# Kernel tuning notes

Hardware: AMD Instinct MI355X
Metric: run time of the kernel (lower is better)

## Reference

```python
import jax, jax.numpy as jnp
import numpy as np

N = 50000        # nodes
E = 300000       # edges
D_IN = 256
D_H = 256
D_OUT = 64       # num classes
L = 3            # num GAT layers
G = 500          # num graphs in batch
NEG_SLOPE = 0.2


def setup_inputs() -> dict:
    key = jax.random.key(0)
    ks = jax.random.split(key, 12)
    x = jax.random.normal(ks[0], (N, D_IN), dtype=jnp.float32)
    edge_index = jax.random.randint(ks[1], (2, E), 0, N, dtype=jnp.int64)
    batch = jnp.sort(jax.random.randint(ks[2], (N,), 0, G, dtype=jnp.int64))
    # GAT layer params (all layers same width since D_IN == D_H)
    Ws = jax.random.normal(ks[3], (L, D_H, D_H), dtype=jnp.float32) * 0.05
    atts = jax.random.normal(ks[4], (L, 2 * D_H, 1), dtype=jnp.float32) * 0.05
    bs = jnp.zeros((L, D_H), dtype=jnp.float32)
    # post_mp: Linear(D_H,D_H) -> Dropout(0) -> Linear(D_H,D_OUT)
    pW1 = jax.random.normal(ks[5], (D_H, D_H), dtype=jnp.float32) * 0.05
    pb1 = jnp.zeros((D_H,), dtype=jnp.float32)
    pW2 = jax.random.normal(ks[6], (D_OUT, D_H), dtype=jnp.float32) * 0.05
    pb2 = jnp.zeros((D_OUT,), dtype=jnp.float32)
    return dict(x=x, edge_index=edge_index, batch=batch, Ws=Ws, atts=atts,
                bs=bs, pW1=pW1, pb1=pb1, pW2=pW2, pb2=pb2)


def _gat_layer(x, W, att, b, src, dst):
    h = x @ W.T                                   # [N, D_H] (lin, no bias)
    xi = h[dst]                                   # target features  [E, D_H]
    xj = h[src]                                   # source features  [E, D_H]
    e = jnp.concatenate([xi, xj], axis=1) @ att   # [E, 1]
    e = jax.nn.leaky_relu(e[:, 0], NEG_SLOPE)     # [E]
    # segment softmax keyed by destination node
    m = jax.ops.segment_max(e, dst, num_segments=N)
    m = jnp.where(jnp.isfinite(m), m, 0.0)        # empty segments -> 0
    ee = jnp.exp(e - m[dst])
    s = jax.ops.segment_sum(ee, dst, num_segments=N)
    alpha = ee / (s[dst] + 1e-16)                 # [E]
    # weighted scatter-add aggregation (aggr='add'); heads=1, concat view is identity
    out = jax.ops.segment_sum(alpha[:, None] * xj, dst, num_segments=N)
    return out + b


def reference(x, edge_index, batch, Ws, atts, bs, pW1, pb1, pW2, pb2):
    src = edge_index[0]
    dst = edge_index[1]
    for l in range(L):
        x = _gat_layer(x, Ws[l], atts[l], bs[l], src, dst)
    # Dropout(p=0) is identity
    x = jax.nn.relu(x)
    g = jax.ops.segment_max(x, batch, num_segments=G)   # global_max_pool [G, D_H]
    h = g @ pW1.T + pb1
    out = h @ pW2.T + pb2
    return jax.nn.log_softmax(out, axis=1)
```

## Files before the change

### kernel.cpp

```cpp
#include <hip/hip_runtime.h>
#include <math.h>

#define NEG_SLOPE 0.2f

typedef __attribute__((ext_vector_type(8))) short s16x8;
typedef __attribute__((ext_vector_type(4))) float f32x4;
typedef unsigned short ushort_t;
typedef unsigned int uint_t;

__device__ inline ushort_t f2bf(float f) {
    unsigned u = __float_as_uint(f);
    unsigned r = (u + 0x7fff + ((u >> 16) & 1)) >> 16;
    return (ushort_t)r;
}
__device__ inline float bf2f(ushort_t u) {
    return __uint_as_float(((unsigned)u) << 16);
}

__global__ __launch_bounds__(256) void cvt_kernel(const float* __restrict__ in,
        ushort_t* __restrict__ out, int n4) {
    int i = blockIdx.x * 256 + threadIdx.x;
    if (i < n4) {
        float4 v = ((const float4*)in)[i];
        ushort4 o;
        o.x = f2bf(v.x); o.y = f2bf(v.y); o.z = f2bf(v.z); o.w = f2bf(v.w);
        ((ushort4*)out)[i] = o;
    }
}

__global__ void deg_kernel(const int* __restrict__ ei, int* __restrict__ deg, int E) {
    int e = blockIdx.x * blockDim.x + threadIdx.x;
    if (e < E) atomicAdd(&deg[ei[E + e]], 1);
}

__global__ __launch_bounds__(1024) void scan1(const int* __restrict__ deg,
        int* __restrict__ tscan, int* __restrict__ bsum, int n) {
    __shared__ int ws[16];
    int t = threadIdx.x;
    int gi = blockIdx.x * 1024 + t;
    int v = (gi < n) ? deg[gi] : 0;
    int lane = t & 63, w = t >> 6;
    int s = v;
#pragma unroll
    for (int off = 1; off < 64; off <<= 1) {
        int u = __shfl_up(s, off);
        if (lane >= off) s += u;
    }
    if (lane == 63) ws[w] = s;
    __syncthreads();
    if (w == 0) {
        int x = (lane < 16) ? ws[lane] : 0;
#pragma unroll
        for (int off = 1; off < 16; off <<= 1) {
            int u = __shfl_up(x, off);
            if (lane >= off) x += u;
        }
        if (lane < 16) ws[lane] = x;
    }
    __syncthreads();
    int woff = (w > 0) ? ws[w - 1] : 0;
    if (gi < n) tscan[gi] = woff + s - v;
    if (t == 1023) bsum[blockIdx.x] = woff + s;
}

__global__ void scan2(const int* __restrict__ bsum, int* __restrict__ boff,
                      int nb, int* __restrict__ total_out) {
    int lane = threadIdx.x;
    int v = (lane < nb) ? bsum[lane] : 0;
    int s = v;
#pragma unroll
    for (int off = 1; off < 64; off <<= 1) {
        int u = __shfl_up(s, off);
        if (lane >= off) s += u;
    }
    if (lane < nb) boff[lane] = s - v;
    if (lane == 63) *total_out = s;
}

__global__ __launch_bounds__(1024) void scan3(const int* __restrict__ tscan,
        const int* __restrict__ boff, int* __restrict__ rowptr,
        int* __restrict__ cursor, int n) {
    int i = blockIdx.x * 1024 + threadIdx.x;
    if (i < n) {
        int v = tscan[i] + boff[blockIdx.x];
        rowptr[i] = v;
        cursor[i] = v;
    }
}

__global__ void scatter_kernel(const int* __restrict__ ei, int* __restrict__ cursor,
                               int* __restrict__ adj, int E) {
    int e = blockIdx.x * blockDim.x + threadIdx.x;
    if (e < E) {
        int d = ei[E + e];
        int pos = atomicAdd(&cursor[d], 1);
        adj[pos] = ei[e];
    }
}

__global__ __launch_bounds__(256) void gemm_bf16(const ushort_t* __restrict__ A,
        const ushort_t* __restrict__ B, ushort_t* __restrict__ C,
        const float* __restrict__ att, float* __restrict__ a_dst,
        float* __restrict__ a_src, int n) {
    __shared__ ushort_t As[128 * 32];
    __shared__ ushort_t Bs[128 * 32];
    const int t = threadIdx.x;
    const int lane = t & 63, wid = t >> 6;
    const int wr = wid >> 1, wc = wid & 1;
    const long brow = (long)blockIdx.x * 128;
    const int bcol = blockIdx.y * 128;

    f32x4 acc[4][4] = {};

    const int r0 = wid * 16 + (lane >> 2);
    const int kof = (lane & 3) * 8;
    const int fr = lane & 15, kg = lane >> 4;

    for (int kt = 0; kt < 256; kt += 32) {
        __builtin_amdgcn_global_load_lds(
            (const __attribute__((address_space(1))) void*)(A + (brow + r0) * 256 + kt + kof),
            (__attribute__((address_space(3))) void*)(As + wid * 512 + lane * 8), 16, 0, 0);
        __builtin_amdgcn_global_load_lds(
            (const __attribute__((address_space(1))) void*)(A + (brow + r0 + 64) * 256 + kt + kof),
            (__attribute__((address_space(3))) void*)(As + (wid + 4) * 512 + lane * 8), 16, 0, 0);
        __builtin_amdgcn_global_load_lds(
            (const __attribute__((address_space(1))) void*)(B + (bcol + r0) * 256 + kt + kof),
            (__attribute__((address_space(3))) void*)(Bs + wid * 512 + lane * 8), 16, 0, 0);
        __builtin_amdgcn_global_load_lds(
            (const __attribute__((address_space(1))) void*)(B + (bcol + r0 + 64) * 256 + kt + kof),
            (__attribute__((address_space(3))) void*)(Bs + (wid + 4) * 512 + lane * 8), 16, 0, 0);
        asm volatile("s_waitcnt vmcnt(0)" ::: "memory");
        __syncthreads();

        s16x8 a[4], b[4];
#pragma unroll
        for (int m = 0; m < 4; m++)
            a[m] = *(const s16x8*)(As + (wr * 64 + m * 16 + fr) * 32 + kg * 8);
#pragma unroll
        for (int nn = 0; nn < 4; nn++)
            b[nn] = *(const s16x8*)(Bs + (wc * 64 + nn * 16 + fr) * 32 + kg * 8);
#pragma unroll
        for (int m = 0; m < 4; m++)
#pragma unroll
            for (int nn = 0; nn < 4; nn++)
                acc[m][nn] = __builtin_amdgcn_mfma_f32_16x16x32_bf16(a[m], b[nn], acc[m][nn], 0, 0, 0);
        __syncthreads();
    }

    const int rg = lane >> 4;
    const float* attL = att;
    const float* attR = att + 256;
#pragma unroll
    for (int m = 0; m < 4; m++) {
        long rbase = brow + wr * 64 + m * 16 + rg * 4;
#pragma unroll
        for (int r = 0; r < 4; r++) {
            long row = rbase + r;
            float sL = 0.f, sR = 0.f;
#pragma unroll
            for (int nn = 0; nn < 4; nn++) {
                int col = bcol + wc * 64 + nn * 16 + fr;
                float v = acc[m][nn][r];
                C[row * 256 + col] = f2bf(v);
                sL = fmaf(v, attL[col], sL);
                sR = fmaf(v, attR[col], sR);
            }
#pragma unroll
            for (int off = 8; off; off >>= 1) {
                sL += __shfl_xor(sL, off);
                sR += __shfl_xor(sR, off);
            }
            if (fr == 0 && row < n) {
                atomicAdd(&a_dst[row], sL);
                atomicAdd(&a_src[row], sR);
            }
        }
    }
}

__global__ __launch_bounds__(256) void gat_agg(const ushort_t* __restrict__ H,
        const float* __restrict__ a_dst, const float* __restrict__ a_src,
        const int* __restrict__ rowptr, const int* __restrict__ adj,
        const float* __restrict__ bias, ushort_t* __restrict__ OUTbf, int n) {
    int w = threadIdx.x >> 6, lane = threadIdx.x & 63;
    int node = blockIdx.x * 4 + w;
    if (node >= n) return;
    int beg = rowptr[node], end = rowptr[node + 1];
    float ai = a_dst[node];

    float m = -3.4e38f;
    for (int j = beg + lane; j < end; j += 64) {
        float e = ai + a_src[adj[j]];
        e = (e > 0.f) ? e : NEG_SLOPE * e;
        m = fmaxf(m, e);
    }
#pragma unroll
    for (int off = 32; off; off >>= 1) m = fmaxf(m, __shfl_xor(m, off));

    const int g = lane >> 4, fl = lane & 15;
    float ssum = 0.f;
    float acc[16];
#pragma unroll
    for (int k = 0; k < 16; k++) acc[k] = 0.f;

    for (int j0 = beg; j0 < end; j0 += 4) {
        int j = j0 + g;
        if (j < end) {
            int sidx = adj[j];
            float tt = ai + a_src[sidx];
            tt = (tt > 0.f) ? tt : NEG_SLOPE * tt;
            float wgt = expf(tt - m);
            ssum += wgt;
            const ushort_t* hp = H + (size_t)sidx * 256 + fl * 16;
            uint4 q0 = *(const uint4*)(hp);
            uint4 q1 = *(const uint4*)(hp + 8);
            uint_t qs[8] = {q0.x, q0.y, q0.z, q0.w, q1.x, q1.y, q1.z, q1.w};
#pragma unroll
            for (int k = 0; k < 8; k++) {
                float flo = __uint_as_float(qs[k] << 16);
                float fhi = __uint_as_float(qs[k] & 0xffff0000u);
                acc[2 * k]     = fmaf(wgt, flo, acc[2 * k]);
                acc[2 * k + 1] = fmaf(wgt, fhi, acc[2 * k + 1]);
            }
        }
    }

#pragma unroll
    for (int k = 0; k < 16; k++) {
        acc[k] += __shfl_xor(acc[k], 16);
        acc[k] += __shfl_xor(acc[k], 32);
    }
    ssum += __shfl_xor(ssum, 16);
    ssum += __shfl_xor(ssum, 32);

    if (g == 0) {
        float inv = 1.f / (ssum + 1e-16f);
        float bv[16];
        *(float4*)&bv[0]  = *(const float4*)(bias + fl * 16);
        *(float4*)&bv[4]  = *(const float4*)(bias + fl * 16 + 4);
        *(float4*)&bv[8]  = *(const float4*)(bias + fl * 16 + 8);
        *(float4*)&bv[12] = *(const float4*)(bias + fl * 16 + 12);
        uint_t ou[8];
#pragma unroll
        for (int k = 0; k < 8; k++) {
            uint_t lo = f2bf(acc[2 * k] * inv + bv[2 * k]);
            uint_t hi = f2bf(acc[2 * k + 1] * inv + bv[2 * k + 1]);
            ou[k] = lo | (hi << 16);
        }
        uint4* op = (uint4*)(OUTbf + (size_t)node * 256 + fl * 16);
        op[0] = make_uint4(ou[0], ou[1], ou[2], ou[3]);
        op[1] = make_uint4(ou[4], ou[5], ou[6], ou[7]);
    }
}

__global__ __launch_bounds__(1024) void pool_kernel(const ushort_t* __restrict__ X,
        const int* __restrict__ batch, float* __restrict__ gbuf, int n) {
    __shared__ float red[4][256];
    int g = blockIdx.x;
    int c = threadIdx.x & 255;
    int rg = threadIdx.x >> 8;
    int lo = 0, hi = n;
    while (lo < hi) { int mid = (lo + hi) >> 1; if (batch[mid] < g) lo = mid + 1; else hi = mid; }
    int start = lo;
    hi = n;
    while (lo < hi) { int mid = (lo + hi) >> 1; if (batch[mid] < g + 1) lo = mid + 1; else hi = mid; }
    int end_ = lo;
    float m = 0.f;
    for (int i = start + rg; i < end_; i += 4)
        m = fmaxf(m, bf2f(X[(size_t)i * 256 + c]));
    red[rg][c] = m;
    __syncthreads();
    if (rg == 0) {
        m = fmaxf(fmaxf(red[0][c], red[1][c]), fmaxf(red[2][c], red[3][c]));
        gbuf[g * 256 + c] = m;
    }
}

__global__ __launch_bounds__(256) void final_kernel(const float* __restrict__ gbuf,
        const float* __restrict__ pW1, const float* __restrict__ pb1,
        const float* __restrict__ pW2, const float* __restrict__ pb2,
        float* __restrict__ out) {
    __shared__ float gl[256];
    __shared__ float h1[256];
    int g = blockIdx.x, t = threadIdx.x;
    gl[t] = gbuf[g * 256 + t];
    __syncthreads();
    float acc = pb1[t];
    for (int k = 0; k < 256; k++) acc = fmaf(gl[k], pW1[t * 256 + k], acc);
    h1[t] = acc;
    __syncthreads();
    if (t < 64) {
        float o = pb2[t];
        for (int k = 0; k < 256; k++) o = fmaf(h1[k], pW2[t * 256 + k], o);
        float mx = o;
#pragma unroll
        for (int off = 32; off; off >>= 1) mx = fmaxf(mx, __shfl_xor(mx, off));
        float ex = expf(o - mx);
        float s = ex;
#pragma unroll
        for (int off = 32; off; off >>= 1) s += __shfl_xor(s, off);
        out[g * 64 + t] = o - mx - logf(s);
    }
}

extern "C" void kernel_launch(void* const* d_in, const int* in_sizes, int n_in,
                              void* d_out, int out_size, void* d_ws, size_t ws_size,
                              hipStream_t stream) {
    const float* x     = (const float*)d_in[0];
    const int*   ei    = (const int*)d_in[1];
    const int*   batch = (const int*)d_in[2];
    const float* Ws    = (const float*)d_in[3];
    const float* atts  = (const float*)d_in[4];
    const float* bs    = (const float*)d_in[5];
    const float* pW1   = (const float*)d_in[6];
    const float* pb1   = (const float*)d_in[7];
    const float* pW2   = (const float*)d_in[8];
    const float* pb2   = (const float*)d_in[9];
    float* out = (float*)d_out;

    const int N = in_sizes[0] / 256;
    const int E = in_sizes[1] / 2;
    const int G = out_size / 64;
    const int L = in_sizes[3] / (256 * 256);
    const int MB = (N + 127) / 128;
    const int Npad = MB * 128;
    const int NT = (N + 1023) / 1024;

    char* ws = (char*)d_ws;
    size_t off = 0;
    auto alloc = [&](size_t bytes) -> char* {
        char* p = ws + off;
        off += (bytes + 255) & ~size_t(255);
        return p;
    };
    ushort_t* Hbf    = (ushort_t*)alloc((size_t)Npad * 256 * 2);
    ushort_t* Xbf    = (ushort_t*)alloc((size_t)Npad * 256 * 2);
    ushort_t* Wbf    = (ushort_t*)alloc((size_t)L * 256 * 256 * 2);
    float*    a_both = (float*)alloc((size_t)2 * N * 4);
    float*    a_dst  = a_both;
    float*    a_src  = a_both + N;
    int*      deg    = (int*)alloc((size_t)N * 4);
    int*      rowptr = (int*)alloc((size_t)(N + 1) * 4);
    int*      cursor = (int*)alloc((size_t)N * 4);
    int*      adj    = (int*)alloc((size_t)E * 4);
    int*      tscan  = (int*)alloc((size_t)N * 4);
    int*      bsum   = (int*)alloc((size_t)64 * 4);
    int*      boff   = (int*)alloc((size_t)64 * 4);
    float*    gbuf   = (float*)alloc((size_t)G * 256 * 4);

    hipMemsetAsync(deg, 0, (size_t)N * 4, stream);
    int eb = (E + 255) / 256;
    deg_kernel<<<eb, 256, 0, stream>>>(ei, deg, E);
    scan1<<<NT, 1024, 0, stream>>>(deg, tscan, bsum, N);
    scan2<<<1, 64, 0, stream>>>(bsum, boff, NT, rowptr + N);
    scan3<<<NT, 1024, 0, stream>>>(tscan, boff, rowptr, cursor, N);
    scatter_kernel<<<eb, 256, 0, stream>>>(ei, cursor, adj, E);

    cvt_kernel<<<(N * 64 + 255) / 256, 256, 0, stream>>>(x, Xbf, N * 64);
    cvt_kernel<<<(L * 16384 + 255) / 256, 256, 0, stream>>>(Ws, Wbf, L * 16384);

    for (int l = 0; l < L; ++l) {
        hipMemsetAsync(a_both, 0, (size_t)2 * N * 4, stream);
        dim3 ggrid(MB, 2);
        gemm_bf16<<<ggrid, 256, 0, stream>>>(Xbf, Wbf + (size_t)l * 65536, Hbf,
                                             atts + (size_t)l * 512, a_dst, a_src, N);
        gat_agg<<<(N + 3) / 4, 256, 0, stream>>>(Hbf, a_dst, a_src, rowptr, adj,
                                                 bs + (size_t)l * 256, Xbf, N);
    }
    pool_kernel<<<G, 1024, 0, stream>>>(Xbf, batch, gbuf, N);
    final_kernel<<<G, 256, 0, stream>>>(gbuf, pW1, pb1, pW2, pb2, out);
}
```

Before: 368.3 us.

## Merge setup launches, drop per-layer memsets, cache edge scores for low-degree nodes

```diff
diff --git a/kernel.cpp b/kernel.cpp
--- a/kernel.cpp
+++ b/kernel.cpp
@@ -17,14 +17,21 @@
     return __uint_as_float(((unsigned)u) << 16);
 }
 
-__global__ __launch_bounds__(256) void cvt_kernel(const float* __restrict__ in,
-        ushort_t* __restrict__ out, int n4) {
+__global__ __launch_bounds__(256) void cvt2_kernel(const float* __restrict__ a,
+        ushort_t* __restrict__ oa, int na4,
+        const float* __restrict__ b, ushort_t* __restrict__ ob, int nb4) {
     int i = blockIdx.x * 256 + threadIdx.x;
-    if (i < n4) {
-        float4 v = ((const float4*)in)[i];
+    if (i < na4) {
+        float4 v = ((const float4*)a)[i];
         ushort4 o;
         o.x = f2bf(v.x); o.y = f2bf(v.y); o.z = f2bf(v.z); o.w = f2bf(v.w);
-        ((ushort4*)out)[i] = o;
+        ((ushort4*)oa)[i] = o;
+    } else if (i - na4 < nb4) {
+        int k = i - na4;
+        float4 v = ((const float4*)b)[k];
+        ushort4 o;
+        o.x = f2bf(v.x); o.y = f2bf(v.y); o.z = f2bf(v.z); o.w = f2bf(v.w);
+        ((ushort4*)ob)[k] = o;
     }
 }
 
@@ -63,28 +70,28 @@
     if (t == 1023) bsum[blockIdx.x] = woff + s;
 }
 
-__global__ void scan2(const int* __restrict__ bsum, int* __restrict__ boff,
-                      int nb, int* __restrict__ total_out) {
-    int lane = threadIdx.x;
-    int v = (lane < nb) ? bsum[lane] : 0;
-    int s = v;
-#pragma unroll
-    for (int off = 1; off < 64; off <<= 1) {
-        int u = __shfl_up(s, off);
-        if (lane >= off) s += u;
-    }
-    if (lane < nb) boff[lane] = s - v;
-    if (lane == 63) *total_out = s;
-}
-
 __global__ __launch_bounds__(1024) void scan3(const int* __restrict__ tscan,
-        const int* __restrict__ boff, int* __restrict__ rowptr,
-        int* __restrict__ cursor, int n) {
-    int i = blockIdx.x * 1024 + threadIdx.x;
+        const int* __restrict__ bsum, const int* __restrict__ deg,
+        int* __restrict__ rowptr, int* __restrict__ cursor, int n, int nb) {
+    __shared__ int sboff;
+    int t = threadIdx.x;
+    if (t < 64) {
+        int v = (t < nb) ? bsum[t] : 0;
+        int s = v;
+#pragma unroll
+        for (int off = 1; off < 64; off <<= 1) {
+            int u = __shfl_up(s, off);
+            if (t >= off) s += u;
+        }
+        if (t == (int)blockIdx.x) sboff = s - v;
+    }
+    __syncthreads();
+    int i = blockIdx.x * 1024 + t;
     if (i < n) {
-        int v = tscan[i] + boff[blockIdx.x];
+        int v = tscan[i] + sboff;
         rowptr[i] = v;
         cursor[i] = v;
+        if (i == n - 1) rowptr[n] = v + deg[i];
     }
 }
 
@@ -186,41 +193,77 @@
     int node = blockIdx.x * 4 + w;
     if (node >= n) return;
     int beg = rowptr[node], end = rowptr[node + 1];
+    int degree = end - beg;
     float ai = a_dst[node];
-
-    float m = -3.4e38f;
-    for (int j = beg + lane; j < end; j += 64) {
-        float e = ai + a_src[adj[j]];
-        e = (e > 0.f) ? e : NEG_SLOPE * e;
-        m = fmaxf(m, e);
-    }
-#pragma unroll
-    for (int off = 32; off; off >>= 1) m = fmaxf(m, __shfl_xor(m, off));
 
     const int g = lane >> 4, fl = lane & 15;
     float ssum = 0.f;
     float acc[16];
 #pragma unroll
     for (int k = 0; k < 16; k++) acc[k] = 0.f;
-
-    for (int j0 = beg; j0 < end; j0 += 4) {
-        int j = j0 + g;
-        if (j < end) {
-            int sidx = adj[j];
-            float tt = ai + a_src[sidx];
-            tt = (tt > 0.f) ? tt : NEG_SLOPE * tt;
-            float wgt = expf(tt - m);
-            ssum += wgt;
-            const ushort_t* hp = H + (size_t)sidx * 256 + fl * 16;
-            uint4 q0 = *(const uint4*)(hp);
-            uint4 q1 = *(const uint4*)(hp + 8);
-            uint_t qs[8] = {q0.x, q0.y, q0.z, q0.w, q1.x, q1.y, q1.z, q1.w};
-#pragma unroll
-            for (int k = 0; k < 8; k++) {
-                float flo = __uint_as_float(qs[k] << 16);
-                float fhi = __uint_as_float(qs[k] & 0xffff0000u);
-                acc[2 * k]     = fmaf(wgt, flo, acc[2 * k]);
-                acc[2 * k + 1] = fmaf(wgt, fhi, acc[2 * k + 1]);
+    float m;
+
+    if (degree <= 64) {
+        int sidx_c = 0;
+        float e_c = -3.4e38f;
+        if (lane < degree) {
+            sidx_c = adj[beg + lane];
+            float tt = ai + a_src[sidx_c];
+            e_c = (tt > 0.f) ? tt : NEG_SLOPE * tt;
+        }
+        m = e_c;
+#pragma unroll
+        for (int off = 32; off; off >>= 1) m = fmaxf(m, __shfl_xor(m, off));
+
+        for (int j0 = 0; j0 < degree; j0 += 4) {
+            int j = j0 + g;
+            if (j < degree) {
+                float ej = __shfl(e_c, j);
+                int sj = __shfl(sidx_c, j);
+                float wgt = expf(ej - m);
+                ssum += wgt;
+                const ushort_t* hp = H + (size_t)sj * 256 + fl * 16;
+                uint4 q0 = *(const uint4*)(hp);
+                uint4 q1 = *(const uint4*)(hp + 8);
+                uint_t qs[8] = {q0.x, q0.y, q0.z, q0.w, q1.x, q1.y, q1.z, q1.w};
+#pragma unroll
+                for (int k = 0; k < 8; k++) {
+                    float flo = __uint_as_float(qs[k] << 16);
+                    float fhi = __uint_as_float(qs[k] & 0xffff0000u);
+                    acc[2 * k]     = fmaf(wgt, flo, acc[2 * k]);
+                    acc[2 * k + 1] = fmaf(wgt, fhi, acc[2 * k + 1]);
+                }
+            }
+        }
+    } else {
+        m = -3.4e38f;
+        for (int j = beg + lane; j < end; j += 64) {
+            float e = ai + a_src[adj[j]];
+            e = (e > 0.f) ? e : NEG_SLOPE * e;
+            m = fmaxf(m, e);
+        }
+#pragma unroll
+        for (int off = 32; off; off >>= 1) m = fmaxf(m, __shfl_xor(m, off));
+
+        for (int j0 = beg; j0 < end; j0 += 4) {
+            int j = j0 + g;
+            if (j < end) {
+                int sidx = adj[j];
+                float tt = ai + a_src[sidx];
+                tt = (tt > 0.f) ? tt : NEG_SLOPE * tt;
+                float wgt = expf(tt - m);
+                ssum += wgt;
+                const ushort_t* hp = H + (size_t)sidx * 256 + fl * 16;
+                uint4 q0 = *(const uint4*)(hp);
+                uint4 q1 = *(const uint4*)(hp + 8);
+                uint_t qs[8] = {q0.x, q0.y, q0.z, q0.w, q1.x, q1.y, q1.z, q1.w};
+#pragma unroll
+                for (int k = 0; k < 8; k++) {
+                    float flo = __uint_as_float(qs[k] << 16);
+                    float fhi = __uint_as_float(qs[k] & 0xffff0000u);
+                    acc[2 * k]     = fmaf(wgt, flo, acc[2 * k]);
+                    acc[2 * k + 1] = fmaf(wgt, fhi, acc[2 * k + 1]);
+                }
             }
         }
     }
@@ -336,31 +379,31 @@
     ushort_t* Hbf    = (ushort_t*)alloc((size_t)Npad * 256 * 2);
     ushort_t* Xbf    = (ushort_t*)alloc((size_t)Npad * 256 * 2);
     ushort_t* Wbf    = (ushort_t*)alloc((size_t)L * 256 * 256 * 2);
-    float*    a_both = (float*)alloc((size_t)2 * N * 4);
-    float*    a_dst  = a_both;
-    float*    a_src  = a_both + N;
+    char*     zbeg   = ws + off;
     int*      deg    = (int*)alloc((size_t)N * 4);
+    float*    a_all  = (float*)alloc((size_t)L * 2 * N * 4);
+    size_t    zlen   = (size_t)((ws + off) - zbeg);
     int*      rowptr = (int*)alloc((size_t)(N + 1) * 4);
     int*      cursor = (int*)alloc((size_t)N * 4);
     int*      adj    = (int*)alloc((size_t)E * 4);
     int*      tscan  = (int*)alloc((size_t)N * 4);
     int*      bsum   = (int*)alloc((size_t)64 * 4);
-    int*      boff   = (int*)alloc((size_t)64 * 4);
     float*    gbuf   = (float*)alloc((size_t)G * 256 * 4);
 
-    hipMemsetAsync(deg, 0, (size_t)N * 4, stream);
+    hipMemsetAsync(zbeg, 0, zlen, stream);
+
     int eb = (E + 255) / 256;
     deg_kernel<<<eb, 256, 0, stream>>>(ei, deg, E);
     scan1<<<NT, 1024, 0, stream>>>(deg, tscan, bsum, N);
-    scan2<<<1, 64, 0, stream>>>(bsum, boff, NT, rowptr + N);
-    scan3<<<NT, 1024, 0, stream>>>(tscan, boff, rowptr, cursor, N);
+    scan3<<<NT, 1024, 0, stream>>>(tscan, bsum, deg, rowptr, cursor, N, NT);
     scatter_kernel<<<eb, 256, 0, stream>>>(ei, cursor, adj, E);
 
-    cvt_kernel<<<(N * 64 + 255) / 256, 256, 0, stream>>>(x, Xbf, N * 64);
-    cvt_kernel<<<(L * 16384 + 255) / 256, 256, 0, stream>>>(Ws, Wbf, L * 16384);
+    int na4 = N * 64, nb4 = L * 16384;
+    cvt2_kernel<<<(na4 + nb4 + 255) / 256, 256, 0, stream>>>(x, Xbf, na4, Ws, Wbf, nb4);
 
     for (int l = 0; l < L; ++l) {
-        hipMemsetAsync(a_both, 0, (size_t)2 * N * 4, stream);
+        float* a_dst = a_all + (size_t)l * 2 * N;
+        float* a_src = a_dst + N;
         dim3 ggrid(MB, 2);
         gemm_bf16<<<ggrid, 256, 0, stream>>>(Xbf, Wbf + (size_t)l * 65536, Hbf,
                                              atts + (size_t)l * 512, a_dst, a_src, N);
```

Result: faster. 351.6 us (-4.5%).
